# Performance work log

Hardware: AMD Instinct MI355X
Metric: run time of the kernel (lower is better)

Reference implementation:

```python
import jax, jax.numpy as jnp
import numpy as np

B, N, DIM = 4, 1024, 512
H, DH = 8, 64
INNER = H * DH
MLP = 2048
EPS = 1e-5


def layernorm(x, g, b):
    m = x.mean(-1, keepdims=True)
    v = ((x - m) ** 2).mean(-1, keepdims=True)
    return (x - m) / jnp.sqrt(v + EPS) * g + b


def setup_inputs() -> dict:
    key = jax.random.key(0)
    ks = jax.random.split(key, 12)
    s = 0.02
    return {
        "q": jax.random.normal(ks[0], (B, N, DIM), jnp.float32),
        "k": jax.random.normal(ks[1], (B, N, DIM), jnp.float32),
        "v": jax.random.normal(ks[2], (B, N, DIM), jnp.float32),
        "Win": jax.random.normal(ks[3], (INNER, DIM), jnp.float32) * s,
        "Wout": jax.random.normal(ks[4], (DIM, INNER), jnp.float32) * s,
        "bout": jnp.zeros((DIM,), jnp.float32),
        "g1": jnp.ones((DIM,), jnp.float32),
        "b1n": jnp.zeros((DIM,), jnp.float32),
        "g2": jnp.ones((DIM,), jnp.float32),
        "b2n": jnp.zeros((DIM,), jnp.float32),
        "Wup": jax.random.normal(ks[5], (MLP, DIM), jnp.float32) * s,
        "bup": jnp.zeros((MLP,), jnp.float32),
        "Wdn": jax.random.normal(ks[6], (DIM, MLP), jnp.float32) * s,
        "bdn": jnp.zeros((DIM,), jnp.float32),
        "wp_W1": jax.random.normal(ks[7], (DH, 2 * DH), jnp.float32) * s,
        "wp_b1": jnp.zeros((DH,), jnp.float32),
        "wp_g": jnp.ones((DH,), jnp.float32),
        "wp_b": jnp.zeros((DH,), jnp.float32),
        "wp_W2": jax.random.normal(ks[8], (3, DH), jnp.float32) * s,
        "wp_b2": jnp.zeros((3,), jnp.float32),
        "num_heads": H,
        "dim_head": DH,
        "mlp_dim": MLP,
    }


def reference(q, k, v, Win, Wout, bout, g1, b1n, g2, b2n, Wup, bup, Wdn, bdn,
              wp_W1, wp_b1, wp_g, wp_b, wp_W2, wp_b2, num_heads, dim_head, mlp_dim):
    b, n, _ = q.shape

    def split_heads(x):  # [b,n,dim] -> [h,b,n,d]
        f = x @ Win.T
        return f.reshape(b, n, num_heads, dim_head).transpose(2, 0, 1, 3)

    fq = split_heads(layernorm(q, g1, b1n))
    fk = split_heads(layernorm(k, g1, b1n))
    fv = split_heads(layernorm(v, g1, b1n))

    # cosine similarity component
    dots = jnp.einsum('hbnd,hbmd->hbnm', fq, fk)
    nq = jnp.linalg.norm(fq, axis=-1)  # [h,b,n]
    nk = jnp.linalg.norm(fk, axis=-1)  # [h,b,m]
    cosine_sim = dots / (nq[..., :, None] * nk[..., None, :])

    # mean-centered covariance component
    qc = fq - fq.mean(-1, keepdims=True)
    kc = fk - fk.mean(-1, keepdims=True)
    cov_component = jnp.einsum('hbnd,hbmd->hbnm', qc, kc) / dim_head

    # variance outer-product component (torch.var -> unbiased, ddof=1)
    qv = jnp.var(fq, axis=-1, ddof=1)  # [h,b,n]
    kv = jnp.var(fk, axis=-1, ddof=1)  # [h,b,m]
    var_component = qv[..., :, None] * kv[..., None, :] / dim_head

    # dynamic per-head mixing weights
    qg = fq.mean(axis=(1, 2))  # [h,d]
    kg = fk.mean(axis=(1, 2))
    feats = jnp.concatenate([qg, kg], axis=-1)  # [h,2d]
    h1 = jax.nn.relu(layernorm(feats @ wp_W1.T + wp_b1, wp_g, wp_b))
    w = jax.nn.softmax(h1 @ wp_W2.T + wp_b2, axis=-1)  # [h,3]
    cw = w[:, 0][:, None, None, None]
    covw = w[:, 1][:, None, None, None]
    vw = w[:, 2][:, None, None, None]

    scores = cw * cosine_sim + covw * cov_component + vw * var_component
    out = jnp.einsum('hbnm,hbmd->hbnd', scores, fv)
    out = out.transpose(1, 2, 0, 3).reshape(b, n, num_heads * dim_head)
    attn = out @ Wout.T + bout

    q2 = q + attn
    x = layernorm(q2, g2, b2n)
    y = jax.nn.gelu(x @ Wup.T + bup, approximate=False) @ Wdn.T + bdn
    return q2 + y
```

## Files before the change

kernel.cpp:

```cpp
#include <hip/hip_runtime.h>
#include <math.h>

#define EPS 1e-5f
#define ROWS 4096

typedef __attribute__((ext_vector_type(8))) short short8;
typedef __attribute__((ext_vector_type(4))) float floatx4;

__device__ inline short f2bf(float f) {
    unsigned u = __builtin_bit_cast(unsigned, f);
    unsigned r = (u + 0x7fffu + ((u >> 16) & 1u)) >> 16;
    return (short)r;
}

__global__ __launch_bounds__(256) void lnconv(
    const float* __restrict__ x0, const float* __restrict__ x1,
    const float* __restrict__ x2, const float* __restrict__ g,
    const float* __restrict__ bb, short* __restrict__ out) {
    int tensor = blockIdx.y;
    const float* x = tensor == 0 ? x0 : (tensor == 1 ? x1 : x2);
    int t = threadIdx.x;
    int row = blockIdx.x * 4 + (t >> 6);
    int col = (t & 63) * 8;
    const float* xr = x + (size_t)row * 512 + col;
    float4 v0 = *(const float4*)xr;
    float4 v1 = *(const float4*)(xr + 4);
    float s = v0.x + v0.y + v0.z + v0.w + v1.x + v1.y + v1.z + v1.w;
    float sq = v0.x * v0.x + v0.y * v0.y + v0.z * v0.z + v0.w * v0.w +
               v1.x * v1.x + v1.y * v1.y + v1.z * v1.z + v1.w * v1.w;
#pragma unroll
    for (int off = 32; off; off >>= 1) {
        s += __shfl_xor(s, off);
        sq += __shfl_xor(sq, off);
    }
    float m = s * (1.f / 512.f);
    float rstd = rsqrtf(sq * (1.f / 512.f) - m * m + EPS);
    float4 g0 = *(const float4*)(g + col);
    float4 g1 = *(const float4*)(g + col + 4);
    float4 b0 = *(const float4*)(bb + col);
    float4 b1 = *(const float4*)(bb + col + 4);
    short8 o;
    o[0] = f2bf((v0.x - m) * rstd * g0.x + b0.x);
    o[1] = f2bf((v0.y - m) * rstd * g0.y + b0.y);
    o[2] = f2bf((v0.z - m) * rstd * g0.z + b0.z);
    o[3] = f2bf((v0.w - m) * rstd * g0.w + b0.w);
    o[4] = f2bf((v1.x - m) * rstd * g1.x + b1.x);
    o[5] = f2bf((v1.y - m) * rstd * g1.y + b1.y);
    o[6] = f2bf((v1.z - m) * rstd * g1.z + b1.z);
    o[7] = f2bf((v1.w - m) * rstd * g1.w + b1.w);
    *(short8*)(out + (size_t)(tensor * 4096 + row) * 512 + col) = o;
}

__global__ void wconv(const float* __restrict__ w0, const float* __restrict__ w1,
                      const float* __restrict__ w2, const float* __restrict__ w3,
                      short* __restrict__ o0, short* __restrict__ o1,
                      short* __restrict__ o2, short* __restrict__ o3) {
    int y = blockIdx.y;
    const float* src = y == 0 ? w0 : (y == 1 ? w1 : (y == 2 ? w2 : w3));
    short* dst = y == 0 ? o0 : (y == 1 ? o1 : (y == 2 ? o2 : o3));
    int n = (y < 2) ? 262144 : 1048576;
    int idx = (blockIdx.x * 256 + threadIdx.x) * 8;
    if (idx < n) {
        float4 v0 = *(const float4*)(src + idx);
        float4 v1 = *(const float4*)(src + idx + 4);
        short8 o;
        o[0] = f2bf(v0.x); o[1] = f2bf(v0.y); o[2] = f2bf(v0.z); o[3] = f2bf(v0.w);
        o[4] = f2bf(v1.x); o[5] = f2bf(v1.y); o[6] = f2bf(v1.z); o[7] = f2bf(v1.w);
        *(short8*)(dst + idx) = o;
    }
}

template <int TM, int TN, int EPI, bool OUT_BF16>
__global__ __launch_bounds__(256) void mfma_gemm_nt(
    const short* __restrict__ A, const short* __restrict__ B,
    void* __restrict__ C, int M, int N, int K,
    const float* __restrict__ bias, const float* __restrict__ resid) {
    constexpr int FI = TM / 32;
    constexpr int FJ = TN / 32;
    __shared__ short As[TM * 32];
    __shared__ short Bs[TN * 32];
    int t = threadIdx.x;
    int m0 = blockIdx.y * TM, n0 = blockIdx.x * TN;
    int w = t >> 6, lane = t & 63;
    int wm = (w & 1) * (TM / 2), wn = (w >> 1) * (TN / 2);
    floatx4 acc[FI][FJ];
#pragma unroll
    for (int i = 0; i < FI; ++i)
#pragma unroll
        for (int j = 0; j < FJ; ++j) acc[i][j] = (floatx4){0.f, 0.f, 0.f, 0.f};

    int arow = t >> 2, acol = (t & 3) * 8;
    const short* Ag = A + (size_t)(m0 + arow) * K + acol;
    const short* Bg = B + (size_t)(n0 + arow) * K + acol;
    int ldsbase = w * 1024;

    for (int k0 = 0; k0 < K; k0 += 32) {
        __syncthreads();
#pragma unroll
        for (int u = 0; u < TM / 64; ++u)
            __builtin_amdgcn_global_load_lds(
                (const __attribute__((address_space(1))) void*)(Ag + (size_t)u * 64 * K + k0),
                (__attribute__((address_space(3))) void*)((char*)As + u * 4096 + ldsbase),
                16, 0, 0);
#pragma unroll
        for (int u = 0; u < TN / 64; ++u)
            __builtin_amdgcn_global_load_lds(
                (const __attribute__((address_space(1))) void*)(Bg + (size_t)u * 64 * K + k0),
                (__attribute__((address_space(3))) void*)((char*)Bs + u * 4096 + ldsbase),
                16, 0, 0);
        __syncthreads();
        int krow = (lane >> 4) * 8;
        short8 af[FI], bf[FJ];
#pragma unroll
        for (int i = 0; i < FI; ++i)
            af[i] = *(const short8*)&As[(wm + i * 16 + (lane & 15)) * 32 + krow];
#pragma unroll
        for (int j = 0; j < FJ; ++j)
            bf[j] = *(const short8*)&Bs[(wn + j * 16 + (lane & 15)) * 32 + krow];
#pragma unroll
        for (int i = 0; i < FI; ++i)
#pragma unroll
            for (int j = 0; j < FJ; ++j)
                acc[i][j] = __builtin_amdgcn_mfma_f32_16x16x32_bf16(
                    af[i], bf[j], acc[i][j], 0, 0, 0);
    }

    int col = lane & 15, rbase = (lane >> 4) * 4;
#pragma unroll
    for (int i = 0; i < FI; ++i) {
#pragma unroll
        for (int j = 0; j < FJ; ++j) {
            int gcol = n0 + wn + j * 16 + col;
#pragma unroll
            for (int r = 0; r < 4; ++r) {
                int grow = m0 + wm + i * 16 + rbase + r;
                float v = acc[i][j][r];
                if (EPI == 2) v += bias[gcol] + resid[(size_t)grow * N + gcol];
                if (EPI == 3) {
                    v += bias[gcol];
                    v = 0.5f * v * (1.f + erff(v * 0.70710678118654752f));
                }
                if (OUT_BF16)
                    ((short*)C)[(size_t)grow * N + gcol] = f2bf(v);
                else
                    ((float*)C)[(size_t)grow * N + gcol] = v;
            }
        }
    }
}

__global__ void head_stats2(const float* __restrict__ fq, const float* __restrict__ fk,
                            float* __restrict__ S) {
    int row = blockIdx.x;
    int y = blockIdx.y;
    const float* f = y ? fk : fq;
    float* base = S + (size_t)y * 98304;
    int t = threadIdx.x;
    int h = t >> 6, lane = t & 63;
    float v = f[(size_t)row * 512 + t];
    float s = v, sq = v * v;
#pragma unroll
    for (int off = 32; off; off >>= 1) {
        s += __shfl_xor(s, off);
        sq += __shfl_xor(sq, off);
    }
    if (lane == 0) {
        float m = s * (1.f / 64.f);
        int idx = h * ROWS + row;
        base[idx] = m;
        base[32768 + idx] = rsqrtf(sq);
        base[65536 + idx] = (sq - 64.f * m * m) * (1.f / 63.f);
    }
}

__global__ void zero_k(float* __restrict__ p, int n) {
    int i = blockIdx.x * blockDim.x + threadIdx.x;
    if (i < n) p[i] = 0.f;
}

__global__ void colmean(const float* __restrict__ fq, const float* __restrict__ fk,
                        float* __restrict__ qg, float* __restrict__ kg) {
    int tensor = blockIdx.y;
    const float* f = tensor ? fk : fq;
    float* o = tensor ? kg : qg;
    int col = threadIdx.x;
    int r0 = blockIdx.x * 32;
    float s = 0.f;
    for (int r = 0; r < 32; ++r) s += f[(size_t)(r0 + r) * 512 + col];
    atomicAdd(&o[col], s * (1.f / 4096.f));
}

__global__ void policy_mlp(const float* __restrict__ qg, const float* __restrict__ kg,
                           const float* __restrict__ W1, const float* __restrict__ b1,
                           const float* __restrict__ g, const float* __restrict__ bb,
                           const float* __restrict__ W2, const float* __restrict__ b2,
                           float* __restrict__ wmix) {
    int h = blockIdx.x, j = threadIdx.x;
    float acc = 0.f;
    const float* w1r = W1 + j * 128;
    for (int i = 0; i < 64; ++i) acc += qg[h * 64 + i] * w1r[i];
    for (int i = 0; i < 64; ++i) acc += kg[h * 64 + i] * w1r[64 + i];
    acc += b1[j];
    float s = acc, sq = acc * acc;
#pragma unroll
    for (int off = 32; off; off >>= 1) {
        s += __shfl_xor(s, off);
        sq += __shfl_xor(sq, off);
    }
    float m = s * (1.f / 64.f);
    float var = sq * (1.f / 64.f) - m * m;
    float xh = (acc - m) * rsqrtf(var + EPS) * g[j] + bb[j];
    float r = fmaxf(xh, 0.f);
    float l[3];
#pragma unroll
    for (int c = 0; c < 3; ++c) {
        float p = r * W2[c * 64 + j];
#pragma unroll
        for (int off = 32; off; off >>= 1) p += __shfl_xor(p, off);
        l[c] = p + b2[c];
    }
    if (j == 0) {
        float mx = fmaxf(l[0], fmaxf(l[1], l[2]));
        float e0 = expf(l[0] - mx), e1 = expf(l[1] - mx), e2 = expf(l[2] - mx);
        float inv = 1.f / (e0 + e1 + e2);
        wmix[h * 3 + 0] = e0 * inv;
        wmix[h * 3 + 1] = e1 * inv;
        wmix[h * 3 + 2] = e2 * inv;
    }
}

__global__ __launch_bounds__(256) void ksideP(
    const float* __restrict__ fk, const float* __restrict__ fv,
    const float* __restrict__ rnk, const float* __restrict__ kvv,
    const float* __restrict__ mk, float* __restrict__ Mpart) {
    int hb = blockIdx.x;
    int chunk = blockIdx.y;
    int h = hb >> 2, b = hb & 3;
    __shared__ float fkt[2048], fvt[2048];
    __shared__ float rs[32], kvs[32], mks[32];
    int t = threadIdx.x;
    int td = t >> 4, te = t & 15;
    float m1[4][4] = {}, m2[4][4] = {};
    float skv = 0.f, smk = 0.f;
    int mstart = chunk * 128;
    for (int m0 = mstart; m0 < mstart + 128; m0 += 32) {
        __syncthreads();
#pragma unroll
        for (int u = 0; u < 2; ++u) {
            int idx = u * 1024 + t * 4;
            int mm = idx >> 6, d = idx & 63;
            size_t grow = (size_t)(b * 1024 + m0 + mm) * 512 + h * 64 + d;
            *(float4*)&fkt[idx] = *(const float4*)&fk[grow];
            *(float4*)&fvt[idx] = *(const float4*)&fv[grow];
        }
        if (t < 32) {
            int sidx = h * ROWS + b * 1024 + m0 + t;
            rs[t] = rnk[sidx];
            kvs[t] = kvv[sidx];
            mks[t] = mk[sidx];
        }
        __syncthreads();
        for (int mi = 0; mi < 32; ++mi) {
            float r = rs[mi];
            float4 kq = *(const float4*)&fkt[mi * 64 + td * 4];
            float4 vq = *(const float4*)&fvt[mi * 64 + te * 4];
            float kr[4] = {kq.x, kq.y, kq.z, kq.w};
            float vr[4] = {vq.x, vq.y, vq.z, vq.w};
#pragma unroll
            for (int i = 0; i < 4; ++i) {
                float kv_ = kr[i], krr = kv_ * r;
#pragma unroll
                for (int j = 0; j < 4; ++j) {
                    m2[i][j] += kv_ * vr[j];
                    m1[i][j] += krr * vr[j];
                }
            }
            if (t < 64) {
                skv += kvs[mi] * fvt[mi * 64 + t];
                smk += mks[mi] * fvt[mi * 64 + t];
            }
        }
    }
    float* base = Mpart + (size_t)(chunk * 32 + hb) * 8320;
#pragma unroll
    for (int i = 0; i < 4; ++i)
#pragma unroll
        for (int j = 0; j < 4; ++j) {
            base[(td * 4 + i) * 64 + te * 4 + j] = m1[i][j];
            base[4096 + (td * 4 + i) * 64 + te * 4 + j] = m2[i][j];
        }
    if (t < 64) {
        base[8192 + t] = skv;
        base[8256 + t] = smk;
    }
}

__global__ void reduceM(const float* __restrict__ Mpart, float* __restrict__ Mbuf) {
    int i = blockIdx.x * 256 + threadIdx.x;
    if (i < 32 * 8320) {
        float s = 0.f;
#pragma unroll
        for (int c = 0; c < 8; ++c) s += Mpart[(size_t)c * 266240 + i];
        Mbuf[i] = s;
    }
}

__global__ __launch_bounds__(256) void qside(
    const float* __restrict__ fq, const float* __restrict__ Mbuf,
    const float* __restrict__ rnq, const float* __restrict__ mq,
    const float* __restrict__ qv, const float* __restrict__ wmix,
    short* __restrict__ attn_out) {
    int ntile = blockIdx.x, hb = blockIdx.y;
    int h = hb >> 2, b = hb & 3;
    __shared__ float M1s[4096], M2s[4096], fqt[4096];
    __shared__ float Skvs[64], Smks[64], rnqs[64], mqs[64], qvs[64];
    int t = threadIdx.x;
    const float* base = Mbuf + (size_t)hb * 8320;
#pragma unroll
    for (int u = 0; u < 4; ++u) {
        int idx = t * 4 + u * 1024;
        *(float4*)&M1s[idx] = *(const float4*)&base[idx];
        *(float4*)&M2s[idx] = *(const float4*)&base[4096 + idx];
    }
    int n0 = ntile * 64;
#pragma unroll
    for (int u = 0; u < 4; ++u) {
        int idx = t * 4 + u * 1024;
        int r = idx >> 6, d = idx & 63;
        *(float4*)&fqt[idx] = *(const float4*)&fq[(size_t)(b * 1024 + n0 + r) * 512 + h * 64 + d];
    }
    if (t < 64) {
        Skvs[t] = base[8192 + t];
        Smks[t] = base[8256 + t];
        int sidx = h * ROWS + b * 1024 + n0 + t;
        rnqs[t] = rnq[sidx];
        mqs[t] = mq[sidx];
        qvs[t] = qv[sidx];
    }
    __syncthreads();
    float cw = wmix[h * 3 + 0], covw = wmix[h * 3 + 1], vw = wmix[h * 3 + 2];
    int e = t & 63, rq = t >> 6;
    float a1[16] = {}, a2[16] = {};
    for (int d4 = 0; d4 < 64; d4 += 4) {
        float md1[4], md2[4];
#pragma unroll
        for (int dd = 0; dd < 4; ++dd) {
            md1[dd] = M1s[(d4 + dd) * 64 + e];
            md2[dd] = M2s[(d4 + dd) * 64 + e];
        }
#pragma unroll
        for (int i = 0; i < 16; ++i) {
            float4 f = *(const float4*)&fqt[(rq * 16 + i) * 64 + d4];
            a1[i] += f.x * md1[0] + f.y * md1[1] + f.z * md1[2] + f.w * md1[3];
            a2[i] += f.x * md2[0] + f.y * md2[1] + f.z * md2[2] + f.w * md2[3];
        }
    }
    float c2 = covw * (1.f / 64.f), c3 = vw * (1.f / 64.f);
#pragma unroll
    for (int i = 0; i < 16; ++i) {
        int rr = rq * 16 + i;
        float v = cw * rnqs[rr] * a1[i] + c2 * a2[i] + c3 * qvs[rr] * Skvs[e] -
                  covw * mqs[rr] * Smks[e];
        attn_out[(size_t)(b * 1024 + n0 + rr) * 512 + h * 64 + e] = f2bf(v);
    }
}

extern "C" void kernel_launch(void* const* d_in, const int* in_sizes, int n_in,
                              void* d_out, int out_size, void* d_ws, size_t ws_size,
                              hipStream_t stream) {
    const float* q = (const float*)d_in[0];
    const float* k = (const float*)d_in[1];
    const float* v = (const float*)d_in[2];
    const float* Win = (const float*)d_in[3];
    const float* Wout = (const float*)d_in[4];
    const float* bout = (const float*)d_in[5];
    const float* g1 = (const float*)d_in[6];
    const float* b1n = (const float*)d_in[7];
    const float* g2 = (const float*)d_in[8];
    const float* b2n = (const float*)d_in[9];
    const float* Wup = (const float*)d_in[10];
    const float* bup = (const float*)d_in[11];
    const float* Wdn = (const float*)d_in[12];
    const float* bdn = (const float*)d_in[13];
    const float* wpW1 = (const float*)d_in[14];
    const float* wpb1 = (const float*)d_in[15];
    const float* wpg = (const float*)d_in[16];
    const float* wpb = (const float*)d_in[17];
    const float* wpW2 = (const float*)d_in[18];
    const float* wpb2 = (const float*)d_in[19];
    float* out = (float*)d_out;

    float* wsf = (float*)d_ws;
    float* fq = wsf;
    float* fk = wsf + 2097152;
    float* fv = wsf + 2 * 2097152;
    short* hmid = (short*)wsf;
    short* qkvln = (short*)(wsf + 6291456);
    float* Mpart = wsf + 6291456;
    short* attnbf = (short*)(wsf + 6291456);
    short* x2bf = (short*)(wsf + 6291456 + 1048576);
    short* Winbf = (short*)(wsf + 9437184);
    short* Woutbf = (short*)(wsf + 9437184 + 131072);
    short* Wupbf = (short*)(wsf + 9437184 + 262144);
    short* Wdnbf = (short*)(wsf + 9437184 + 262144 + 524288);
    float* S = wsf + 10747904;
    float* qg = S + 196608;
    float* kg = qg + 512;
    float* Mbuf = kg + 512;
    float* wmix = Mbuf + 266240;
    float* mqS = S, *rnqS = S + 32768, *qvS = S + 65536;
    float* mkS = S + 98304, *rnkS = S + 131072, *kvS = S + 163840;

    wconv<<<dim3(512, 4), 256, 0, stream>>>(Win, Wout, Wup, Wdn,
                                            Winbf, Woutbf, Wupbf, Wdnbf);
    lnconv<<<dim3(1024, 3), 256, 0, stream>>>(q, k, v, g1, b1n, qkvln);
    zero_k<<<4, 256, 0, stream>>>(qg, 1024);

    mfma_gemm_nt<64, 128, 0, false><<<dim3(4, 192), 256, 0, stream>>>(
        qkvln, Winbf, fq, 12288, 512, 512, nullptr, nullptr);

    head_stats2<<<dim3(4096, 2), 512, 0, stream>>>(fq, fk, S);
    colmean<<<dim3(128, 2), 512, 0, stream>>>(fq, fk, qg, kg);
    policy_mlp<<<8, 64, 0, stream>>>(qg, kg, wpW1, wpb1, wpg, wpb, wpW2, wpb2, wmix);

    ksideP<<<dim3(32, 8), 256, 0, stream>>>(fk, fv, rnkS, kvS, mkS, Mpart);
    reduceM<<<1040, 256, 0, stream>>>(Mpart, Mbuf);
    qside<<<dim3(16, 32), 256, 0, stream>>>(fq, Mbuf, rnqS, mqS, qvS, wmix, attnbf);

    mfma_gemm_nt<64, 64, 2, false><<<dim3(8, 64), 256, 0, stream>>>(
        attnbf, Woutbf, out, 4096, 512, 512, bout, q);

    lnconv<<<dim3(1024, 1), 256, 0, stream>>>(out, out, out, g2, b2n, x2bf);
    mfma_gemm_nt<64, 128, 3, true><<<dim3(16, 64), 256, 0, stream>>>(
        x2bf, Wupbf, hmid, 4096, 2048, 512, bup, nullptr);
    mfma_gemm_nt<64, 128, 2, false><<<dim3(4, 64), 256, 0, stream>>>(
        hmid, Wdnbf, out, 4096, 512, 2048, bdn, out);
}
```

Before: 271.4 us.

## Fuse prep kernels, store QKV projections in bf16, compute policy means algebraically

Merges weight conversion, input layernorm and zeroing into a single prep launch. The QKV projection now writes bf16 instead of fp32, and downstream stats, k-side and q-side kernels read bf16. The per-head means are computed from column means of the normalized inputs multiplied by Win inside a fused policy kernel, replacing the column means of the full projection. The GEMM now stages K=64 per barrier, the k-side kernel uses more chunks, and the down-projection tile shrinks. Together these cut launches, memory traffic and syncs, at the cost of storing projections at lower precision.

```diff
diff --git a/kernel.cpp b/kernel.cpp
--- a/kernel.cpp
+++ b/kernel.cpp
@@ -12,13 +12,79 @@
     unsigned r = (u + 0x7fffu + ((u >> 16) & 1u)) >> 16;
     return (short)r;
 }
-
-__global__ __launch_bounds__(256) void lnconv(
-    const float* __restrict__ x0, const float* __restrict__ x1,
-    const float* __restrict__ x2, const float* __restrict__ g,
+__device__ inline float bf2f(short s) {
+    unsigned u = ((unsigned)(unsigned short)s) << 16;
+    return __builtin_bit_cast(float, u);
+}
+
+__global__ __launch_bounds__(256) void prep(
+    const float* __restrict__ Win, const float* __restrict__ Wout,
+    const float* __restrict__ Wup, const float* __restrict__ Wdn,
+    short* __restrict__ Winbf, short* __restrict__ Woutbf,
+    short* __restrict__ Wupbf, short* __restrict__ Wdnbf,
+    const float* __restrict__ q, const float* __restrict__ k,
+    const float* __restrict__ v, const float* __restrict__ g,
+    const float* __restrict__ bb, short* __restrict__ qkvln,
+    float* __restrict__ zbase) {
+    int bid = blockIdx.x;
+    int t = threadIdx.x;
+    if (bid < 1280) {
+        int lb = bid;
+        const float* src;
+        short* dst;
+        if (lb < 128) { src = Win; dst = Winbf; }
+        else if (lb < 256) { lb -= 128; src = Wout; dst = Woutbf; }
+        else if (lb < 768) { lb -= 256; src = Wup; dst = Wupbf; }
+        else { lb -= 768; src = Wdn; dst = Wdnbf; }
+        int idx = (lb * 256 + t) * 8;
+        float4 v0 = *(const float4*)(src + idx);
+        float4 v1 = *(const float4*)(src + idx + 4);
+        short8 o;
+        o[0] = f2bf(v0.x); o[1] = f2bf(v0.y); o[2] = f2bf(v0.z); o[3] = f2bf(v0.w);
+        o[4] = f2bf(v1.x); o[5] = f2bf(v1.y); o[6] = f2bf(v1.z); o[7] = f2bf(v1.w);
+        *(short8*)(dst + idx) = o;
+    } else if (bid < 4352) {
+        int lb = bid - 1280;
+        int tensor = lb >> 10;
+        const float* x = tensor == 0 ? q : (tensor == 1 ? k : v);
+        int row = (lb & 1023) * 4 + (t >> 6);
+        int col = (t & 63) * 8;
+        const float* xr = x + (size_t)row * 512 + col;
+        float4 v0 = *(const float4*)xr;
+        float4 v1 = *(const float4*)(xr + 4);
+        float s = v0.x + v0.y + v0.z + v0.w + v1.x + v1.y + v1.z + v1.w;
+        float sq = v0.x * v0.x + v0.y * v0.y + v0.z * v0.z + v0.w * v0.w +
+                   v1.x * v1.x + v1.y * v1.y + v1.z * v1.z + v1.w * v1.w;
+#pragma unroll
+        for (int off = 32; off; off >>= 1) {
+            s += __shfl_xor(s, off);
+            sq += __shfl_xor(sq, off);
+        }
+        float m = s * (1.f / 512.f);
+        float rstd = rsqrtf(sq * (1.f / 512.f) - m * m + EPS);
+        float4 g0 = *(const float4*)(g + col);
+        float4 g1 = *(const float4*)(g + col + 4);
+        float4 b0 = *(const float4*)(bb + col);
+        float4 b1 = *(const float4*)(bb + col + 4);
+        short8 o;
+        o[0] = f2bf((v0.x - m) * rstd * g0.x + b0.x);
+        o[1] = f2bf((v0.y - m) * rstd * g0.y + b0.y);
+        o[2] = f2bf((v0.z - m) * rstd * g0.z + b0.z);
+        o[3] = f2bf((v0.w - m) * rstd * g0.w + b0.w);
+        o[4] = f2bf((v1.x - m) * rstd * g1.x + b1.x);
+        o[5] = f2bf((v1.y - m) * rstd * g1.y + b1.y);
+        o[6] = f2bf((v1.z - m) * rstd * g1.z + b1.z);
+        o[7] = f2bf((v1.w - m) * rstd * g1.w + b1.w);
+        *(short8*)(qkvln + (size_t)(tensor * 4096 + row) * 512 + col) = o;
+    } else {
+        float4 z = {0.f, 0.f, 0.f, 0.f};
+        *(float4*)(zbase + t * 4) = z;
+    }
+}
+
+__global__ __launch_bounds__(256) void lnsingle(
+    const float* __restrict__ x, const float* __restrict__ g,
     const float* __restrict__ bb, short* __restrict__ out) {
-    int tensor = blockIdx.y;
-    const float* x = tensor == 0 ? x0 : (tensor == 1 ? x1 : x2);
     int t = threadIdx.x;
     int row = blockIdx.x * 4 + (t >> 6);
     int col = (t & 63) * 8;
@@ -48,26 +114,7 @@
     o[5] = f2bf((v1.y - m) * rstd * g1.y + b1.y);
     o[6] = f2bf((v1.z - m) * rstd * g1.z + b1.z);
     o[7] = f2bf((v1.w - m) * rstd * g1.w + b1.w);
-    *(short8*)(out + (size_t)(tensor * 4096 + row) * 512 + col) = o;
-}
-
-__global__ void wconv(const float* __restrict__ w0, const float* __restrict__ w1,
-                      const float* __restrict__ w2, const float* __restrict__ w3,
-                      short* __restrict__ o0, short* __restrict__ o1,
-                      short* __restrict__ o2, short* __restrict__ o3) {
-    int y = blockIdx.y;
-    const float* src = y == 0 ? w0 : (y == 1 ? w1 : (y == 2 ? w2 : w3));
-    short* dst = y == 0 ? o0 : (y == 1 ? o1 : (y == 2 ? o2 : o3));
-    int n = (y < 2) ? 262144 : 1048576;
-    int idx = (blockIdx.x * 256 + threadIdx.x) * 8;
-    if (idx < n) {
-        float4 v0 = *(const float4*)(src + idx);
-        float4 v1 = *(const float4*)(src + idx + 4);
-        short8 o;
-        o[0] = f2bf(v0.x); o[1] = f2bf(v0.y); o[2] = f2bf(v0.z); o[3] = f2bf(v0.w);
-        o[4] = f2bf(v1.x); o[5] = f2bf(v1.y); o[6] = f2bf(v1.z); o[7] = f2bf(v1.w);
-        *(short8*)(dst + idx) = o;
-    }
+    *(short8*)(out + (size_t)row * 512 + col) = o;
 }
 
 template <int TM, int TN, int EPI, bool OUT_BF16>
@@ -77,8 +124,8 @@
     const float* __restrict__ bias, const float* __restrict__ resid) {
     constexpr int FI = TM / 32;
     constexpr int FJ = TN / 32;
-    __shared__ short As[TM * 32];
-    __shared__ short Bs[TN * 32];
+    __shared__ short As[2 * TM * 32];
+    __shared__ short Bs[2 * TN * 32];
     int t = threadIdx.x;
     int m0 = blockIdx.y * TM, n0 = blockIdx.x * TN;
     int w = t >> 6, lane = t & 63;
@@ -94,35 +141,41 @@
     const short* Bg = B + (size_t)(n0 + arow) * K + acol;
     int ldsbase = w * 1024;
 
-    for (int k0 = 0; k0 < K; k0 += 32) {
+    for (int k0 = 0; k0 < K; k0 += 64) {
         __syncthreads();
 #pragma unroll
-        for (int u = 0; u < TM / 64; ++u)
-            __builtin_amdgcn_global_load_lds(
-                (const __attribute__((address_space(1))) void*)(Ag + (size_t)u * 64 * K + k0),
-                (__attribute__((address_space(3))) void*)((char*)As + u * 4096 + ldsbase),
-                16, 0, 0);
-#pragma unroll
-        for (int u = 0; u < TN / 64; ++u)
-            __builtin_amdgcn_global_load_lds(
-                (const __attribute__((address_space(1))) void*)(Bg + (size_t)u * 64 * K + k0),
-                (__attribute__((address_space(3))) void*)((char*)Bs + u * 4096 + ldsbase),
-                16, 0, 0);
+        for (int u = 0; u < 2; ++u) {
+#pragma unroll
+            for (int r = 0; r < TM / 64; ++r)
+                __builtin_amdgcn_global_load_lds(
+                    (const __attribute__((address_space(1))) void*)(Ag + (size_t)r * 64 * K + k0 + 32 * u),
+                    (__attribute__((address_space(3))) void*)((char*)As + u * TM * 64 + r * 4096 + ldsbase),
+                    16, 0, 0);
+#pragma unroll
+            for (int r = 0; r < TN / 64; ++r)
+                __builtin_amdgcn_global_load_lds(
+                    (const __attribute__((address_space(1))) void*)(Bg + (size_t)r * 64 * K + k0 + 32 * u),
+                    (__attribute__((address_space(3))) void*)((char*)Bs + u * TN * 64 + r * 4096 + ldsbase),
+                    16, 0, 0);
+        }
         __syncthreads();
         int krow = (lane >> 4) * 8;
-        short8 af[FI], bf[FJ];
-#pragma unroll
-        for (int i = 0; i < FI; ++i)
-            af[i] = *(const short8*)&As[(wm + i * 16 + (lane & 15)) * 32 + krow];
-#pragma unroll
-        for (int j = 0; j < FJ; ++j)
-            bf[j] = *(const short8*)&Bs[(wn + j * 16 + (lane & 15)) * 32 + krow];
-#pragma unroll
-        for (int i = 0; i < FI; ++i)
+#pragma unroll
+        for (int u = 0; u < 2; ++u) {
+            short8 af[FI], bf[FJ];
+#pragma unroll
+            for (int i = 0; i < FI; ++i)
+                af[i] = *(const short8*)&As[u * TM * 32 + (wm + i * 16 + (lane & 15)) * 32 + krow];
 #pragma unroll
             for (int j = 0; j < FJ; ++j)
-                acc[i][j] = __builtin_amdgcn_mfma_f32_16x16x32_bf16(
-                    af[i], bf[j], acc[i][j], 0, 0, 0);
+                bf[j] = *(const short8*)&Bs[u * TN * 32 + (wn + j * 16 + (lane & 15)) * 32 + krow];
+#pragma unroll
+            for (int i = 0; i < FI; ++i)
+#pragma unroll
+                for (int j = 0; j < FJ; ++j)
+                    acc[i][j] = __builtin_amdgcn_mfma_f32_16x16x32_bf16(
+                        af[i], bf[j], acc[i][j], 0, 0, 0);
+        }
     }
 
     int col = lane & 15, rbase = (lane >> 4) * 4;
@@ -149,15 +202,14 @@
     }
 }
 
-__global__ void head_stats2(const float* __restrict__ fq, const float* __restrict__ fk,
-                            float* __restrict__ S) {
+__global__ void head_stats2(const short* __restrict__ fqkv, float* __restrict__ S) {
     int row = blockIdx.x;
     int y = blockIdx.y;
-    const float* f = y ? fk : fq;
+    const short* f = fqkv + (size_t)y * 4096 * 512;
     float* base = S + (size_t)y * 98304;
     int t = threadIdx.x;
     int h = t >> 6, lane = t & 63;
-    float v = f[(size_t)row * 512 + t];
+    float v = bf2f(f[(size_t)row * 512 + t]);
     float s = v, sq = v * v;
 #pragma unroll
     for (int off = 32; off; off >>= 1) {
@@ -173,33 +225,49 @@
     }
 }
 
-__global__ void zero_k(float* __restrict__ p, int n) {
-    int i = blockIdx.x * blockDim.x + threadIdx.x;
-    if (i < n) p[i] = 0.f;
-}
-
-__global__ void colmean(const float* __restrict__ fq, const float* __restrict__ fk,
-                        float* __restrict__ qg, float* __restrict__ kg) {
-    int tensor = blockIdx.y;
-    const float* f = tensor ? fk : fq;
-    float* o = tensor ? kg : qg;
+__global__ void colmean_ln(const short* __restrict__ qkvln,
+                           float* __restrict__ qgl, float* __restrict__ kgl) {
+    int y = blockIdx.y;
+    const short* f = qkvln + (size_t)y * 4096 * 512;
+    float* o = y ? kgl : qgl;
     int col = threadIdx.x;
     int r0 = blockIdx.x * 32;
     float s = 0.f;
-    for (int r = 0; r < 32; ++r) s += f[(size_t)(r0 + r) * 512 + col];
+    for (int r = 0; r < 32; ++r) s += bf2f(f[(size_t)(r0 + r) * 512 + col]);
     atomicAdd(&o[col], s * (1.f / 4096.f));
 }
 
-__global__ void policy_mlp(const float* __restrict__ qg, const float* __restrict__ kg,
-                           const float* __restrict__ W1, const float* __restrict__ b1,
-                           const float* __restrict__ g, const float* __restrict__ bb,
-                           const float* __restrict__ W2, const float* __restrict__ b2,
-                           float* __restrict__ wmix) {
-    int h = blockIdx.x, j = threadIdx.x;
+__global__ __launch_bounds__(512) void policy_fused(
+    const float* __restrict__ qgl, const float* __restrict__ kgl,
+    const short* __restrict__ Winbf,
+    const float* __restrict__ W1, const float* __restrict__ b1,
+    const float* __restrict__ g, const float* __restrict__ bb,
+    const float* __restrict__ W2, const float* __restrict__ b2,
+    float* __restrict__ wmix) {
+    __shared__ float qgl_s[512], kgl_s[512], qg_s[512], kg_s[512];
+    int t = threadIdx.x;
+    qgl_s[t] = qgl[t];
+    kgl_s[t] = kgl[t];
+    __syncthreads();
+    const short* wr = Winbf + (size_t)t * 512;
+    float accq = 0.f, acck = 0.f;
+    for (int i = 0; i < 512; i += 8) {
+        short8 w8 = *(const short8*)(wr + i);
+#pragma unroll
+        for (int u = 0; u < 8; ++u) {
+            float wv = bf2f(w8[u]);
+            accq += qgl_s[i + u] * wv;
+            acck += kgl_s[i + u] * wv;
+        }
+    }
+    qg_s[t] = accq;
+    kg_s[t] = acck;
+    __syncthreads();
+    int h = t >> 6, j = t & 63;
     float acc = 0.f;
     const float* w1r = W1 + j * 128;
-    for (int i = 0; i < 64; ++i) acc += qg[h * 64 + i] * w1r[i];
-    for (int i = 0; i < 64; ++i) acc += kg[h * 64 + i] * w1r[64 + i];
+    for (int i = 0; i < 64; ++i) acc += qg_s[h * 64 + i] * w1r[i];
+    for (int i = 0; i < 64; ++i) acc += kg_s[h * 64 + i] * w1r[64 + i];
     acc += b1[j];
     float s = acc, sq = acc * acc;
 #pragma unroll
@@ -230,9 +298,11 @@
 }
 
 __global__ __launch_bounds__(256) void ksideP(
-    const float* __restrict__ fk, const float* __restrict__ fv,
+    const short* __restrict__ fqkv,
     const float* __restrict__ rnk, const float* __restrict__ kvv,
     const float* __restrict__ mk, float* __restrict__ Mpart) {
+    const short* fk = fqkv + (size_t)4096 * 512;
+    const short* fv = fqkv + (size_t)2 * 4096 * 512;
     int hb = blockIdx.x;
     int chunk = blockIdx.y;
     int h = hb >> 2, b = hb & 3;
@@ -242,16 +312,20 @@
     int td = t >> 4, te = t & 15;
     float m1[4][4] = {}, m2[4][4] = {};
     float skv = 0.f, smk = 0.f;
-    int mstart = chunk * 128;
-    for (int m0 = mstart; m0 < mstart + 128; m0 += 32) {
+    int mstart = chunk * 64;
+    for (int m0 = mstart; m0 < mstart + 64; m0 += 32) {
         __syncthreads();
-#pragma unroll
-        for (int u = 0; u < 2; ++u) {
-            int idx = u * 1024 + t * 4;
-            int mm = idx >> 6, d = idx & 63;
-            size_t grow = (size_t)(b * 1024 + m0 + mm) * 512 + h * 64 + d;
-            *(float4*)&fkt[idx] = *(const float4*)&fk[grow];
-            *(float4*)&fvt[idx] = *(const float4*)&fv[grow];
+        {
+            int row8 = t >> 3, col8 = (t & 7) * 8;
+            size_t grow = (size_t)(b * 1024 + m0 + row8) * 512 + h * 64 + col8;
+            short8 ks = *(const short8*)&fk[grow];
+            short8 vs = *(const short8*)&fv[grow];
+            int idx = t * 8;
+#pragma unroll
+            for (int u = 0; u < 8; ++u) {
+                fkt[idx + u] = bf2f(ks[u]);
+                fvt[idx + u] = bf2f(vs[u]);
+            }
         }
         if (t < 32) {
             int sidx = h * ROWS + b * 1024 + m0 + t;
@@ -300,16 +374,17 @@
     if (i < 32 * 8320) {
         float s = 0.f;
 #pragma unroll
-        for (int c = 0; c < 8; ++c) s += Mpart[(size_t)c * 266240 + i];
+        for (int c = 0; c < 16; ++c) s += Mpart[(size_t)c * 266240 + i];
         Mbuf[i] = s;
     }
 }
 
 __global__ __launch_bounds__(256) void qside(
-    const float* __restrict__ fq, const float* __restrict__ Mbuf,
+    const short* __restrict__ fqkv, const float* __restrict__ Mbuf,
     const float* __restrict__ rnq, const float* __restrict__ mq,
     const float* __restrict__ qv, const float* __restrict__ wmix,
     short* __restrict__ attn_out) {
+    const short* fq = fqkv;
     int ntile = blockIdx.x, hb = blockIdx.y;
     int h = hb >> 2, b = hb & 3;
     __shared__ float M1s[4096], M2s[4096], fqt[4096];
@@ -324,10 +399,12 @@
     }
     int n0 = ntile * 64;
 #pragma unroll
-    for (int u = 0; u < 4; ++u) {
-        int idx = t * 4 + u * 1024;
+    for (int u = 0; u < 2; ++u) {
+        int idx = u * 2048 + t * 8;
         int r = idx >> 6, d = idx & 63;
-        *(float4*)&fqt[idx] = *(const float4*)&fq[(size_t)(b * 1024 + n0 + r) * 512 + h * 64 + d];
+        short8 qs = *(const short8*)&fq[(size_t)(b * 1024 + n0 + r) * 512 + h * 64 + d];
+#pragma unroll
+        for (int uu = 0; uu < 8; ++uu) fqt[idx + uu] = bf2f(qs[uu]);
     }
     if (t < 64) {
         Skvs[t] = base[8192 + t];
@@ -391,48 +468,46 @@
     float* out = (float*)d_out;
 
     float* wsf = (float*)d_ws;
-    float* fq = wsf;
-    float* fk = wsf + 2097152;
-    float* fv = wsf + 2 * 2097152;
-    short* hmid = (short*)wsf;
-    short* qkvln = (short*)(wsf + 6291456);
-    float* Mpart = wsf + 6291456;
-    short* attnbf = (short*)(wsf + 6291456);
-    short* x2bf = (short*)(wsf + 6291456 + 1048576);
-    short* Winbf = (short*)(wsf + 9437184);
-    short* Woutbf = (short*)(wsf + 9437184 + 131072);
-    short* Wupbf = (short*)(wsf + 9437184 + 262144);
-    short* Wdnbf = (short*)(wsf + 9437184 + 262144 + 524288);
-    float* S = wsf + 10747904;
-    float* qg = S + 196608;
-    float* kg = qg + 512;
-    float* Mbuf = kg + 512;
-    float* wmix = Mbuf + 266240;
+    short* fqkv = (short*)wsf;
+    short* qkvln = (short*)(wsf + 4000000);
+    short* attnbf = (short*)(wsf + 8000000);
+    short* x2bf = (short*)(wsf + 10000000);
+    short* hmid = (short*)(wsf + 12000000);
+    short* Winbf = (short*)(wsf + 17000000);
+    short* Woutbf = Winbf + 262144;
+    short* Wupbf = Woutbf + 262144;
+    short* Wdnbf = Wupbf + 1048576;
+    float* S = wsf + 19000000;
+    float* qgl = S + 196608;
+    float* kgl = qgl + 512;
+    float* wmix = kgl + 512;
+    float* Mbuf = wsf + 19400000;
+    float* Mpart = wsf + 20000000;
     float* mqS = S, *rnqS = S + 32768, *qvS = S + 65536;
     float* mkS = S + 98304, *rnkS = S + 131072, *kvS = S + 163840;
 
-    wconv<<<dim3(512, 4), 256, 0, stream>>>(Win, Wout, Wup, Wdn,
-                                            Winbf, Woutbf, Wupbf, Wdnbf);
-    lnconv<<<dim3(1024, 3), 256, 0, stream>>>(q, k, v, g1, b1n, qkvln);
-    zero_k<<<4, 256, 0, stream>>>(qg, 1024);
-
-    mfma_gemm_nt<64, 128, 0, false><<<dim3(4, 192), 256, 0, stream>>>(
-        qkvln, Winbf, fq, 12288, 512, 512, nullptr, nullptr);
-
-    head_stats2<<<dim3(4096, 2), 512, 0, stream>>>(fq, fk, S);
-    colmean<<<dim3(128, 2), 512, 0, stream>>>(fq, fk, qg, kg);
-    policy_mlp<<<8, 64, 0, stream>>>(qg, kg, wpW1, wpb1, wpg, wpb, wpW2, wpb2, wmix);
-
-    ksideP<<<dim3(32, 8), 256, 0, stream>>>(fk, fv, rnkS, kvS, mkS, Mpart);
+    prep<<<4353, 256, 0, stream>>>(Win, Wout, Wup, Wdn, Winbf, Woutbf, Wupbf,
+                                   Wdnbf, q, k, v, g1, b1n, qkvln, qgl);
+
+    mfma_gemm_nt<64, 128, 0, true><<<dim3(4, 192), 256, 0, stream>>>(
+        qkvln, Winbf, fqkv, 12288, 512, 512, nullptr, nullptr);
+
+    colmean_ln<<<dim3(128, 2), 512, 0, stream>>>(qkvln, qgl, kgl);
+    policy_fused<<<1, 512, 0, stream>>>(qgl, kgl, Winbf, wpW1, wpb1, wpg, wpb,
+                                        wpW2, wpb2, wmix);
+
+    head_stats2<<<dim3(4096, 2), 512, 0, stream>>>(fqkv, S);
+
+    ksideP<<<dim3(32, 16), 256, 0, stream>>>(fqkv, rnkS, kvS, mkS, Mpart);
     reduceM<<<1040, 256, 0, stream>>>(Mpart, Mbuf);
-    qside<<<dim3(16, 32), 256, 0, stream>>>(fq, Mbuf, rnqS, mqS, qvS, wmix, attnbf);
+    qside<<<dim3(16, 32), 256, 0, stream>>>(fqkv, Mbuf, rnqS, mqS, qvS, wmix, attnbf);
 
     mfma_gemm_nt<64, 64, 2, false><<<dim3(8, 64), 256, 0, stream>>>(
         attnbf, Woutbf, out, 4096, 512, 512, bout, q);
 
-    lnconv<<<dim3(1024, 1), 256, 0, stream>>>(out, out, out, g2, b2n, x2bf);
+    lnsingle<<<1024, 256, 0, stream>>>(out, g2, b2n, x2bf);
     mfma_gemm_nt<64, 128, 3, true><<<dim3(16, 64), 256, 0, stream>>>(
         x2bf, Wupbf, hmid, 4096, 2048, 512, bup, nullptr);
-    mfma_gemm_nt<64, 128, 2, false><<<dim3(4, 64), 256, 0, stream>>>(
+    mfma_gemm_nt<64, 64, 2, false><<<dim3(8, 64), 256, 0, stream>>>(
         hmid, Wdnbf, out, 4096, 512, 2048, bdn, out);
 }
```

New measurement: 294.2 us. 8.4% more time.
